# Optimization experiments

Measured on AMD Instinct MI355X. Metric: run time of the kernel, lower is better.

The kernel has to match this reference:

```python
import math
import jax, jax.numpy as jnp
import numpy as np

S = 2  # scale_factor
IN_CH = 256
OFFSET_FACTOR = math.sqrt(128.0 / IN_CH)


def setup_inputs() -> dict:
    key = jax.random.key(0)
    k1, k2, k3 = jax.random.split(key, 3)
    x = jax.random.normal(k1, (4, IN_CH, 128, 128), jnp.float32)
    conv_w = jax.random.normal(k2, (2 * S * S, IN_CH, 1, 1), jnp.float32) * 0.01
    conv_b = jax.random.normal(k3, (2 * S * S,), jnp.float32) * 0.01
    return {"x": x, "conv_w": conv_w, "conv_b": conv_b}


def reference(x, conv_w, conv_b):
    b, c, H, W = x.shape
    s = S
    # 1x1 conv producing per-subpixel (x, y) offsets: [b, 2*s*s, H, W]
    out = jnp.einsum('bchw,oc->bohw', x, conv_w[:, :, 0, 0]) + conv_b[None, :, None, None]
    o1, o2 = jnp.split(out, 2, axis=1)  # each [b, s*s, H, W]
    # sub-pixel bias grid (meshgrid 'xy'): X[i,j]=x[j], Y[i,j]=y[i]
    sub = jnp.arange(0.0, 1.0, 1.0 / s)
    xb, yb = jnp.meshgrid(sub, sub, indexing='xy')  # [s, s]
    xb = xb.reshape(1, -1, 1, 1)
    yb = yb.reshape(1, -1, 1, 1)
    o1 = OFFSET_FACTOR * o1 + jnp.arange(W)[None, None, None, :] + xb  # x coords (pixels)
    o2 = OFFSET_FACTOR * o2 + jnp.arange(H)[None, None, :, None] + yb  # y coords (pixels)
    # [b,2,s,s,H,W] -> [b,2,H,s,W,s] -> [b,2,N], N = s*H*s*W
    off = jnp.stack((o1, o2), axis=1).reshape(b, 2, s, s, H, W)
    off = off.transpose(0, 1, 4, 2, 5, 3).reshape(b, 2, -1)
    xc, yc = off[:, 0], off[:, 1]  # [b, N]
    x0 = jnp.floor(xc)
    y0 = jnp.floor(yc)
    fx = xc - x0
    fy = yc - y0
    x0i = jnp.clip(x0.astype(jnp.int32), 0, W - 1)
    x1i = jnp.clip(x0.astype(jnp.int32) + 1, 0, W - 1)
    y0i = jnp.clip(y0.astype(jnp.int32), 0, H - 1)
    y1i = jnp.clip(y0.astype(jnp.int32) + 1, 0, H - 1)
    bidx = jnp.arange(b)[:, None]

    def gather(yi, xi):
        return x[bidx, :, yi, xi]  # [b, N, c]

    val = (gather(y0i, x0i) * ((1 - fx) * (1 - fy))[..., None]
           + gather(y0i, x1i) * (fx * (1 - fy))[..., None]
           + gather(y1i, x0i) * ((1 - fx) * fy)[..., None]
           + gather(y1i, x1i) * (fx * fy)[..., None])  # [b, N, c]
    return val.transpose(0, 2, 1).reshape(b, c, s * H, s * W)
```

## Files before the change

kernel.cpp:

```cpp
#include <hip/hip_runtime.h>
#include <math.h>

#define BATCH 4
#define C 256
#define H 128
#define W 128
#define HW (H * W)
#define OH 256
#define OW 256
#define KSPLIT 4
#define KCH (C / KSPLIT)
#define SCH 32
#define NCHUNK (C / SCH)
__device__ __constant__ float OFF_FACTOR = 0.70710678118654752f;

typedef float __attribute__((ext_vector_type(2))) f32x2;

__global__ __launch_bounds__(256) void conv_desc_kernel(
    const float* __restrict__ x, const float* __restrict__ cw,
    const float* __restrict__ cb, float2* __restrict__ desc) {
    __shared__ float sw[8 * C];
    __shared__ __align__(16) float red[KSPLIT * 8 * 256];
    int t = threadIdx.x;

    #pragma unroll
    for (int i = 0; i < 8; ++i) sw[i * 256 + t] = cw[i * 256 + t];
    __syncthreads();

    int k = t >> 6;
    int q = t & 63;
    int g4 = blockIdx.x * 64 + q;
    int g = g4 * 4;
    int b = g >> 14;
    int pix = g & (HW - 1);
    const float* xp = x + (size_t)b * C * HW + (size_t)(k * KCH) * HW + pix;

    float4 acc[8];
    #pragma unroll
    for (int o = 0; o < 8; ++o) acc[o] = make_float4(0.f, 0.f, 0.f, 0.f);

    #pragma unroll 8
    for (int c = 0; c < KCH; ++c) {
        float4 v = *(const float4*)(xp + (size_t)c * HW);
        #pragma unroll
        for (int o = 0; o < 8; ++o) {
            float wv = sw[o * C + k * KCH + c];
            acc[o].x += v.x * wv; acc[o].y += v.y * wv;
            acc[o].z += v.z * wv; acc[o].w += v.w * wv;
        }
    }

    #pragma unroll
    for (int o = 0; o < 8; ++o)
        *(float4*)&red[((k * 8 + o) << 8) + (q << 2)] = acc[o];
    __syncthreads();

    int g2 = blockIdx.x * 256 + t;
    int b2 = g2 >> 14;
    int pix2 = g2 & (HW - 1);
    int h2 = pix2 >> 7;
    int w2 = pix2 & (W - 1);

    float s[8];
    #pragma unroll
    for (int o = 0; o < 8; ++o) {
        float a = cb[o];
        #pragma unroll
        for (int kk = 0; kk < KSPLIT; ++kk)
            a += red[((kk * 8 + o) << 8) + t];
        s[o] = a;
    }

    #pragma unroll
    for (int sy = 0; sy < 2; ++sy) {
        int j0 = sy * 2;
        float yb = (float)h2 + 0.5f * (float)sy;
        float xc0 = OFF_FACTOR * s[j0]     + (float)w2;
        float yc0 = OFF_FACTOR * s[4 + j0] + yb;
        float xc1 = OFF_FACTOR * s[j0 + 1] + (float)w2 + 0.5f;
        float yc1 = OFF_FACTOR * s[5 + j0] + yb;
        int p = (b2 * OH + 2 * h2 + sy) * OW + 2 * w2;
        *(float4*)&desc[p] = make_float4(xc0, yc0, xc1, yc1);
    }
}

__global__ __launch_bounds__(256) void sample_kernel(
    const float* __restrict__ x, const float4* __restrict__ desc4,
    float* __restrict__ out) {
    __shared__ __align__(16) float tile[SCH * 4 * W];
    int t = threadIdx.x;
    int lin = blockIdx.x;
    int xcd = lin & 7;
    int i8  = lin >> 3;
    int combo = xcd * 4 + (i8 >> 6);
    int hblk  = i8 & 63;
    int b = combo >> 3;
    int chunk = combo & 7;
    int h0 = hblk * 2;
    int c0 = chunk * SCH;

    const float* xb = x + (size_t)b * C * HW + (size_t)c0 * HW;

    #pragma unroll
    for (int j = 0; j < 16; ++j) {
        int idx = (j * 256 + t) * 4;
        int c   = idx >> 9;
        int i   = (idx >> 7) & 3;
        int col = idx & 127;
        int row = min(max(h0 - 1 + i, 0), H - 1);
        *(float4*)&tile[idx] =
            *(const float4*)(xb + (size_t)c * HW + row * W + col);
    }

    int hr = t >> 7;
    int w  = t & 127;
    int hh = h0 + hr;

    float4 d0 = desc4[(((size_t)b * OH + 2 * hh) * OW + 2 * w) >> 1];
    float4 d1 = desc4[(((size_t)b * OH + 2 * hh + 1) * OW + 2 * w) >> 1];

    int   loff[4][4];
    float wt[4][4];
    bool allok = true;
    float xcs[4] = {d0.x, d0.z, d1.x, d1.z};
    float ycs[4] = {d0.y, d0.w, d1.y, d1.w};
    #pragma unroll
    for (int j = 0; j < 4; ++j) {
        float xc = xcs[j], yc = ycs[j];
        float x0f = floorf(xc), y0f = floorf(yc);
        float fx = xc - x0f, fy = yc - y0f;
        int x0 = (int)x0f, y0 = (int)y0f;
        int x0i = min(max(x0, 0), W - 1), x1i = min(max(x0 + 1, 0), W - 1);
        int y0i = min(max(y0, 0), H - 1), y1i = min(max(y0 + 1, 0), H - 1);
        int iy0 = y0i - h0 + 1, iy1 = y1i - h0 + 1;
        allok = allok && ((unsigned)iy0 <= 3u) && ((unsigned)iy1 <= 3u);
        loff[j][0] = iy0 * W + x0i;  loff[j][1] = iy0 * W + x1i;
        loff[j][2] = iy1 * W + x0i;  loff[j][3] = iy1 * W + x1i;
        wt[j][0] = (1.f - fx) * (1.f - fy); wt[j][1] = fx * (1.f - fy);
        wt[j][2] = (1.f - fx) * fy;         wt[j][3] = fx * fy;
    }

    __syncthreads();

    float* op0 = out + (((size_t)(b * C + c0) * OH + 2 * hh) * OW) + 2 * w;

    if (__all(allok)) {
        #pragma unroll 4
        for (int c = 0; c < SCH; ++c) {
            const float* tl = tile + c * (4 * W);
            float v[4];
            #pragma unroll
            for (int j = 0; j < 4; ++j)
                v[j] = tl[loff[j][0]] * wt[j][0] + tl[loff[j][1]] * wt[j][1] +
                       tl[loff[j][2]] * wt[j][2] + tl[loff[j][3]] * wt[j][3];
            float* op = op0 + (size_t)c * (OH * OW);
            f32x2 r0 = {v[0], v[1]};
            f32x2 r1 = {v[2], v[3]};
            __builtin_nontemporal_store(r0, (f32x2*)op);
            __builtin_nontemporal_store(r1, (f32x2*)(op + OW));
        }
    } else {
        int rebase = (h0 - 1) * W;
        #pragma unroll 2
        for (int c = 0; c < SCH; ++c) {
            const float* pl = xb + (size_t)c * HW;
            float v[4];
            #pragma unroll
            for (int j = 0; j < 4; ++j)
                v[j] = pl[loff[j][0] + rebase] * wt[j][0] +
                       pl[loff[j][1] + rebase] * wt[j][1] +
                       pl[loff[j][2] + rebase] * wt[j][2] +
                       pl[loff[j][3] + rebase] * wt[j][3];
            float* op = op0 + (size_t)c * (OH * OW);
            f32x2 r0 = {v[0], v[1]};
            f32x2 r1 = {v[2], v[3]};
            __builtin_nontemporal_store(r0, (f32x2*)op);
            __builtin_nontemporal_store(r1, (f32x2*)(op + OW));
        }
    }
}

extern "C" void kernel_launch(void* const* d_in, const int* in_sizes, int n_in,
                              void* d_out, int out_size, void* d_ws, size_t ws_size,
                              hipStream_t stream) {
    const float* x  = (const float*)d_in[0];
    const float* cw = (const float*)d_in[1];
    const float* cb = (const float*)d_in[2];
    float* out = (float*)d_out;

    float2* desc = (float2*)d_ws;

    conv_desc_kernel<<<256, 256, 0, stream>>>(x, cw, cb, desc);
    sample_kernel<<<BATCH * (H / 2) * NCHUNK, 256, 0, stream>>>(
        x, (const float4*)desc, out);
}
```

Baseline: 314.8 us.

## Halve channel chunk per sample block and use single-base bilinear offsets

Reduces channels per sampling block from 32 to 16. This doubles the grid, halves shared-memory tile size for higher occupancy, and remaps the block-to-XCD assignment. Also recasts border clamping as a clamped base corner (x0c, y0c) with adjusted fractional weights. Each sample then keeps one offset instead of four, which cuts register pressure and index arithmetic. The cost is more redundant loading of halo rows and descriptors across the extra blocks.

Result: no change. 311.4 us (-1.1%).

```diff
diff --git a/kernel.cpp b/kernel.cpp
--- a/kernel.cpp
+++ b/kernel.cpp
@@ -10,7 +10,7 @@
 #define OW 256
 #define KSPLIT 4
 #define KCH (C / KSPLIT)
-#define SCH 32
+#define SCH 16
 #define NCHUNK (C / SCH)
 __device__ __constant__ float OFF_FACTOR = 0.70710678118654752f;
 
@@ -92,17 +92,17 @@
     int lin = blockIdx.x;
     int xcd = lin & 7;
     int i8  = lin >> 3;
-    int combo = xcd * 4 + (i8 >> 6);
+    int combo = xcd * 8 + (i8 >> 6);
     int hblk  = i8 & 63;
-    int b = combo >> 3;
-    int chunk = combo & 7;
+    int b = combo >> 4;
+    int chunk = combo & 15;
     int h0 = hblk * 2;
     int c0 = chunk * SCH;
 
     const float* xb = x + (size_t)b * C * HW + (size_t)c0 * HW;
 
     #pragma unroll
-    for (int j = 0; j < 16; ++j) {
+    for (int j = 0; j < 8; ++j) {
         int idx = (j * 256 + t) * 4;
         int c   = idx >> 9;
         int i   = (idx >> 7) & 3;
@@ -119,7 +119,7 @@
     float4 d0 = desc4[(((size_t)b * OH + 2 * hh) * OW + 2 * w) >> 1];
     float4 d1 = desc4[(((size_t)b * OH + 2 * hh + 1) * OW + 2 * w) >> 1];
 
-    int   loff[4][4];
+    int   loff[4];
     float wt[4][4];
     bool allok = true;
     float xcs[4] = {d0.x, d0.z, d1.x, d1.z};
@@ -128,14 +128,14 @@
     for (int j = 0; j < 4; ++j) {
         float xc = xcs[j], yc = ycs[j];
         float x0f = floorf(xc), y0f = floorf(yc);
-        float fx = xc - x0f, fy = yc - y0f;
         int x0 = (int)x0f, y0 = (int)y0f;
-        int x0i = min(max(x0, 0), W - 1), x1i = min(max(x0 + 1, 0), W - 1);
-        int y0i = min(max(y0, 0), H - 1), y1i = min(max(y0 + 1, 0), H - 1);
-        int iy0 = y0i - h0 + 1, iy1 = y1i - h0 + 1;
-        allok = allok && ((unsigned)iy0 <= 3u) && ((unsigned)iy1 <= 3u);
-        loff[j][0] = iy0 * W + x0i;  loff[j][1] = iy0 * W + x1i;
-        loff[j][2] = iy1 * W + x0i;  loff[j][3] = iy1 * W + x1i;
+        int x0c = min(max(x0, 0), W - 2);
+        int y0c = min(max(y0, 0), H - 2);
+        float fx = (x0 < 0) ? 0.f : ((x0 > W - 2) ? 1.f : xc - x0f);
+        float fy = (y0 < 0) ? 0.f : ((y0 > H - 2) ? 1.f : yc - y0f);
+        int iy0 = y0c - h0 + 1;
+        allok = allok && ((unsigned)iy0 <= 2u);
+        loff[j] = iy0 * W + x0c;
         wt[j][0] = (1.f - fx) * (1.f - fy); wt[j][1] = fx * (1.f - fy);
         wt[j][2] = (1.f - fx) * fy;         wt[j][3] = fx * fy;
     }
@@ -150,9 +150,13 @@
             const float* tl = tile + c * (4 * W);
             float v[4];
             #pragma unroll
-            for (int j = 0; j < 4; ++j)
-                v[j] = tl[loff[j][0]] * wt[j][0] + tl[loff[j][1]] * wt[j][1] +
-                       tl[loff[j][2]] * wt[j][2] + tl[loff[j][3]] * wt[j][3];
+            for (int j = 0; j < 4; ++j) {
+                int bj = loff[j];
+                float t00 = tl[bj],     t01 = tl[bj + 1];
+                float t10 = tl[bj + W], t11 = tl[bj + W + 1];
+                v[j] = t00 * wt[j][0] + t01 * wt[j][1] +
+                       t10 * wt[j][2] + t11 * wt[j][3];
+            }
             float* op = op0 + (size_t)c * (OH * OW);
             f32x2 r0 = {v[0], v[1]};
             f32x2 r1 = {v[2], v[3]};
@@ -166,11 +170,11 @@
             const float* pl = xb + (size_t)c * HW;
             float v[4];
             #pragma unroll
-            for (int j = 0; j < 4; ++j)
-                v[j] = pl[loff[j][0] + rebase] * wt[j][0] +
-                       pl[loff[j][1] + rebase] * wt[j][1] +
-                       pl[loff[j][2] + rebase] * wt[j][2] +
-                       pl[loff[j][3] + rebase] * wt[j][3];
+            for (int j = 0; j < 4; ++j) {
+                int bj = loff[j] + rebase;
+                v[j] = pl[bj]         * wt[j][0] + pl[bj + 1]     * wt[j][1] +
+                       pl[bj + W]     * wt[j][2] + pl[bj + W + 1] * wt[j][3];
+            }
             float* op = op0 + (size_t)c * (OH * OW);
             f32x2 r0 = {v[0], v[1]};
             f32x2 r1 = {v[2], v[3]};
```
